# Performance work log

Hardware: AMD Instinct MI355X
Metric: run time of the kernel (lower is better)

## Reference

```python
import jax, jax.numpy as jnp
import numpy as np

N_NODES = 100000
FEAT_DIM = 256
EMBED_DIM = 256
BATCH = 50000
NUM_SAMPLE = 25
NAN_FILL = 0.01  # neigh_feats[isnan] = 0.01 in the original


def setup_inputs() -> dict:
    key = jax.random.key(0)
    k1, k2, k3, k4 = jax.random.split(key, 4)
    features = jax.random.normal(k1, (N_NODES, FEAT_DIM), dtype=jnp.float32)
    # Xavier-uniform-ish weight [embed_dim, feat_dim + embed_dim] (gcn=True)
    fan = FEAT_DIM + EMBED_DIM
    bound = float(np.sqrt(6.0 / (EMBED_DIM + fan)))
    weight = jax.random.uniform(k2, (EMBED_DIM, fan), dtype=jnp.float32,
                                minval=-bound, maxval=bound)
    nodes = jax.random.randint(k3, (BATCH,), 0, N_NODES, dtype=jnp.int64)
    neigh_idx = jax.random.randint(k4, (BATCH, NUM_SAMPLE), 0, N_NODES, dtype=jnp.int64)
    return {"features": features, "weight": weight, "nodes": nodes,
            "neigh_idx": neigh_idx}


def reference(features, weight, nodes, neigh_idx):
    # MeanAggregator: gather sampled neighbor features and mean over neighbors
    neigh_feats = features[neigh_idx].mean(axis=1)            # [B, F]
    neigh_feats = jnp.where(jnp.isnan(neigh_feats), NAN_FILL, neigh_feats)
    self_feats = features[nodes]                              # [B, F]
    combined = jnp.concatenate([self_feats, neigh_feats], axis=1)  # [B, F+E]
    # weight.matmul(combined.t()) then ReLU -> [E, B]
    out = jax.nn.relu(jnp.einsum('ef,bf->eb', weight, combined))
    return out
```

## Files before the change

kernel.cpp:

```cpp
#include <hip/hip_runtime.h>
#include <hip/hip_bf16.h>
#include <hip/hip_fp8.h>

#define FEAT    256
#define KDIM    512
#define EMBED   256
#define BATCH   50000
#define NSAMP   25
#define N_NODES 100000
#define NAN_FILL 0.01f

#define NTILE   48
#define LSTRIDE 520

typedef __attribute__((ext_vector_type(8))) short  short8;
typedef __attribute__((ext_vector_type(4))) float  floatx4;
typedef __attribute__((ext_vector_type(4))) unsigned short ushort4v;
typedef __attribute__((ext_vector_type(4))) float  float4v;

__device__ inline unsigned short f2bf(float x) {
    __hip_bfloat16 h = __float2bfloat16(x);
    union { __hip_bfloat16 h; unsigned short u; } c; c.h = h;
    return c.u;
}
__device__ inline unsigned char f2fp8(float x) {
    __hip_fp8_e4m3 t(x);
    return (unsigned char)t.__x;
}
__device__ inline float fp8f(unsigned v) {
    __hip_fp8_e4m3 t; t.__x = (unsigned char)v;
    return (float)t;
}

__global__ __launch_bounds__(256) void fconv8_kernel(
    const float* __restrict__ F, unsigned char* __restrict__ F8)
{
    const size_t i = ((size_t)blockIdx.x * 256 + threadIdx.x) * 8;
    float4v a = *(const float4v*)(F + i);
    float4v b = *(const float4v*)(F + i + 4);
    union { unsigned char c[8]; uint2 v; } o;
    o.c[0] = f2fp8(a[0]); o.c[1] = f2fp8(a[1]); o.c[2] = f2fp8(a[2]); o.c[3] = f2fp8(a[3]);
    o.c[4] = f2fp8(b[0]); o.c[5] = f2fp8(b[1]); o.c[6] = f2fp8(b[2]); o.c[7] = f2fp8(b[3]);
    *(uint2*)(F8 + i) = o.v;
}

__global__ __launch_bounds__(256) void wconv_kernel(
    const float* __restrict__ W, unsigned short* __restrict__ Wb)
{
    const int i = blockIdx.x * 256 + threadIdx.x;
    Wb[i] = f2bf(W[i]);
}

__global__ __launch_bounds__(256, 3) void enc_kernel(
    const float* __restrict__ F,
    const unsigned char* __restrict__ F8,
    const unsigned short* __restrict__ Wb,
    const int* __restrict__ nodes,
    const int* __restrict__ neigh,
    float* __restrict__ out)
{
    __shared__ unsigned short cl[NTILE * LSTRIDE];

    const int lane = threadIdx.x & 63;
    const int wave = threadIdx.x >> 6;
    const int q = lane >> 4;
    const int r = lane & 15;
    const int nbase = blockIdx.x * NTILE;

    for (int it = 0; it < NTILE / 4; ++it) {
        const int li = wave * (NTILE / 4) + it;
        int b = nbase + li;
        if (b >= BATCH) b = BATCH - 1;

        const int node = nodes[b];
        float4v sv = *(const float4v*)(F + (size_t)node * FEAT + lane * 4);

        const int* nb = neigh + (size_t)b * NSAMP;
        float s0 = 0.f, s1 = 0.f, s2 = 0.f, s3 = 0.f;
        #pragma unroll
        for (int j = 0; j < NSAMP; ++j) {
            const int idx = nb[j];
            unsigned wv = *(const unsigned*)(F8 + (size_t)idx * FEAT + lane * 4);
            s0 += fp8f(wv);
            s1 += fp8f(wv >> 8);
            s2 += fp8f(wv >> 16);
            s3 += fp8f(wv >> 24);
        }
        const float inv = 1.0f / NSAMP;
        float m0 = s0 * inv, m1 = s1 * inv, m2 = s2 * inv, m3 = s3 * inv;
        if (m0 != m0) m0 = NAN_FILL;
        if (m1 != m1) m1 = NAN_FILL;
        if (m2 != m2) m2 = NAN_FILL;
        if (m3 != m3) m3 = NAN_FILL;

        unsigned short* row = cl + li * LSTRIDE;
        ushort4v s; s[0] = f2bf(sv[0]); s[1] = f2bf(sv[1]); s[2] = f2bf(sv[2]); s[3] = f2bf(sv[3]);
        *(ushort4v*)(row + lane * 4) = s;
        ushort4v m; m[0] = f2bf(m0); m[1] = f2bf(m1); m[2] = f2bf(m2); m[3] = f2bf(m3);
        *(ushort4v*)(row + FEAT + lane * 4) = m;
    }
    __syncthreads();

    const int mbase = wave * 64;
    const short* Wp = (const short*)Wb;
    const short* cp = (const short*)cl;

    floatx4 acc[4][3] = {};

    for (int k = 0; k < KDIM; k += 32) {
        short8 afr[4], bfr[3];
        #pragma unroll
        for (int mt = 0; mt < 4; ++mt) {
            const short* p = Wp + (size_t)(mbase + mt * 16 + r) * KDIM + k + q * 8;
            afr[mt] = *(const short8*)p;
        }
        #pragma unroll
        for (int nt = 0; nt < 3; ++nt) {
            const short* p = cp + (nt * 16 + r) * LSTRIDE + k + q * 8;
            bfr[nt] = *(const short8*)p;
        }
        #pragma unroll
        for (int mt = 0; mt < 4; ++mt)
            #pragma unroll
            for (int nt = 0; nt < 3; ++nt)
                acc[mt][nt] = __builtin_amdgcn_mfma_f32_16x16x32_bf16(
                    afr[mt], bfr[nt], acc[mt][nt], 0, 0, 0);
    }

    #pragma unroll
    for (int mt = 0; mt < 4; ++mt) {
        #pragma unroll
        for (int nt = 0; nt < 3; ++nt) {
            const int col = nbase + nt * 16 + r;
            if (col < BATCH) {
                #pragma unroll
                for (int i = 0; i < 4; ++i) {
                    const int row = mbase + mt * 16 + q * 4 + i;
                    float v = acc[mt][nt][i];
                    out[(size_t)row * BATCH + col] = v > 0.f ? v : 0.f;
                }
            }
        }
    }
}

extern "C" void kernel_launch(void* const* d_in, const int* in_sizes, int n_in,
                              void* d_out, int out_size, void* d_ws, size_t ws_size,
                              hipStream_t stream) {
    const float* features = (const float*)d_in[0];
    const float* weight   = (const float*)d_in[1];
    const int*   nodes    = (const int*)d_in[2];
    const int*   neigh    = (const int*)d_in[3];
    float* out = (float*)d_out;

    unsigned char* F8  = (unsigned char*)d_ws;
    unsigned short* Wb = (unsigned short*)(F8 + (size_t)N_NODES * FEAT);

    fconv8_kernel<<<(N_NODES * FEAT) / (256 * 8), 256, 0, stream>>>(features, F8);
    wconv_kernel<<<(EMBED * KDIM) / 256, 256, 0, stream>>>(weight, Wb);

    const int nblocks = (BATCH + NTILE - 1) / NTILE;
    enc_kernel<<<nblocks, 256, 0, stream>>>(features, F8, Wb, nodes, neigh, out);
}
```

Before: 256.9 us.

## Fuse conversion kernels, use hardware packed FP8 converts, shrink node tile

The two preprocessing kernels become one launch that converts features to FP8 and the weight to BF16, with vectorized stores. Scalar FP8 encode and decode helpers are replaced by the packed hardware conversion builtins, both when converting features and when summing neighbor rows. The encoder tile shrinks from 48 to 32 nodes per block, and launch bounds request 4 blocks per CU instead of 3 to raise occupancy. The cost is more blocks and more reloads of the weight per node column.

```diff
diff --git a/kernel.cpp b/kernel.cpp
--- a/kernel.cpp
+++ b/kernel.cpp
@@ -1,6 +1,5 @@
 #include <hip/hip_runtime.h>
 #include <hip/hip_bf16.h>
-#include <hip/hip_fp8.h>
 
 #define FEAT    256
 #define KDIM    512
@@ -10,11 +9,15 @@
 #define N_NODES 100000
 #define NAN_FILL 0.01f
 
-#define NTILE   48
+#define NTILE   32
 #define LSTRIDE 520
+
+#define FCONV_BLOCKS 12500
+#define WCONV_BLOCKS 64
 
 typedef __attribute__((ext_vector_type(8))) short  short8;
 typedef __attribute__((ext_vector_type(4))) float  floatx4;
+typedef __attribute__((ext_vector_type(2))) float  float2v;
 typedef __attribute__((ext_vector_type(4))) unsigned short ushort4v;
 typedef __attribute__((ext_vector_type(4))) float  float4v;
 
@@ -23,35 +26,35 @@
     union { __hip_bfloat16 h; unsigned short u; } c; c.h = h;
     return c.u;
 }
-__device__ inline unsigned char f2fp8(float x) {
-    __hip_fp8_e4m3 t(x);
-    return (unsigned char)t.__x;
-}
-__device__ inline float fp8f(unsigned v) {
-    __hip_fp8_e4m3 t; t.__x = (unsigned char)v;
-    return (float)t;
+
+__global__ __launch_bounds__(256) void conv_kernel(
+    const float* __restrict__ F, unsigned char* __restrict__ F8,
+    const float* __restrict__ W, unsigned short* __restrict__ Wb)
+{
+    if (blockIdx.x < FCONV_BLOCKS) {
+        const size_t i = ((size_t)blockIdx.x * 256 + threadIdx.x) * 8;
+        float4v a = *(const float4v*)(F + i);
+        float4v b = *(const float4v*)(F + i + 4);
+        int p0 = 0, p1 = 0;
+        p0 = __builtin_amdgcn_cvt_pk_fp8_f32(a[0], a[1], p0, false);
+        p0 = __builtin_amdgcn_cvt_pk_fp8_f32(a[2], a[3], p0, true);
+        p1 = __builtin_amdgcn_cvt_pk_fp8_f32(b[0], b[1], p1, false);
+        p1 = __builtin_amdgcn_cvt_pk_fp8_f32(b[2], b[3], p1, true);
+        uint2 o; o.x = (unsigned)p0; o.y = (unsigned)p1;
+        *(uint2*)(F8 + i) = o;
+    } else {
+        const size_t i = ((size_t)(blockIdx.x - FCONV_BLOCKS) * 256 + threadIdx.x) * 8;
+        float4v a = *(const float4v*)(W + i);
+        float4v b = *(const float4v*)(W + i + 4);
+        ushort4v o0, o1;
+        o0[0] = f2bf(a[0]); o0[1] = f2bf(a[1]); o0[2] = f2bf(a[2]); o0[3] = f2bf(a[3]);
+        o1[0] = f2bf(b[0]); o1[1] = f2bf(b[1]); o1[2] = f2bf(b[2]); o1[3] = f2bf(b[3]);
+        *(ushort4v*)(Wb + i) = o0;
+        *(ushort4v*)(Wb + i + 4) = o1;
+    }
 }
 
-__global__ __launch_bounds__(256) void fconv8_kernel(
-    const float* __restrict__ F, unsigned char* __restrict__ F8)
-{
-    const size_t i = ((size_t)blockIdx.x * 256 + threadIdx.x) * 8;
-    float4v a = *(const float4v*)(F + i);
-    float4v b = *(const float4v*)(F + i + 4);
-    union { unsigned char c[8]; uint2 v; } o;
-    o.c[0] = f2fp8(a[0]); o.c[1] = f2fp8(a[1]); o.c[2] = f2fp8(a[2]); o.c[3] = f2fp8(a[3]);
-    o.c[4] = f2fp8(b[0]); o.c[5] = f2fp8(b[1]); o.c[6] = f2fp8(b[2]); o.c[7] = f2fp8(b[3]);
-    *(uint2*)(F8 + i) = o.v;
-}
-
-__global__ __launch_bounds__(256) void wconv_kernel(
-    const float* __restrict__ W, unsigned short* __restrict__ Wb)
-{
-    const int i = blockIdx.x * 256 + threadIdx.x;
-    Wb[i] = f2bf(W[i]);
-}
-
-__global__ __launch_bounds__(256, 3) void enc_kernel(
+__global__ __launch_bounds__(256, 4) void enc_kernel(
     const float* __restrict__ F,
     const unsigned char* __restrict__ F8,
     const unsigned short* __restrict__ Wb,
@@ -80,11 +83,10 @@
         #pragma unroll
         for (int j = 0; j < NSAMP; ++j) {
             const int idx = nb[j];
-            unsigned wv = *(const unsigned*)(F8 + (size_t)idx * FEAT + lane * 4);
-            s0 += fp8f(wv);
-            s1 += fp8f(wv >> 8);
-            s2 += fp8f(wv >> 16);
-            s3 += fp8f(wv >> 24);
+            int wv = *(const int*)(F8 + (size_t)idx * FEAT + lane * 4);
+            float2v lo = __builtin_amdgcn_cvt_pk_f32_fp8(wv, false);
+            float2v hi = __builtin_amdgcn_cvt_pk_f32_fp8(wv, true);
+            s0 += lo[0]; s1 += lo[1]; s2 += hi[0]; s3 += hi[1];
         }
         const float inv = 1.0f / NSAMP;
         float m0 = s0 * inv, m1 = s1 * inv, m2 = s2 * inv, m3 = s3 * inv;
@@ -105,24 +107,24 @@
     const short* Wp = (const short*)Wb;
     const short* cp = (const short*)cl;
 
-    floatx4 acc[4][3] = {};
+    floatx4 acc[4][2] = {};
 
     for (int k = 0; k < KDIM; k += 32) {
-        short8 afr[4], bfr[3];
+        short8 afr[4], bfr[2];
         #pragma unroll
         for (int mt = 0; mt < 4; ++mt) {
             const short* p = Wp + (size_t)(mbase + mt * 16 + r) * KDIM + k + q * 8;
             afr[mt] = *(const short8*)p;
         }
         #pragma unroll
-        for (int nt = 0; nt < 3; ++nt) {
+        for (int nt = 0; nt < 2; ++nt) {
             const short* p = cp + (nt * 16 + r) * LSTRIDE + k + q * 8;
             bfr[nt] = *(const short8*)p;
         }
         #pragma unroll
         for (int mt = 0; mt < 4; ++mt)
             #pragma unroll
-            for (int nt = 0; nt < 3; ++nt)
+            for (int nt = 0; nt < 2; ++nt)
                 acc[mt][nt] = __builtin_amdgcn_mfma_f32_16x16x32_bf16(
                     afr[mt], bfr[nt], acc[mt][nt], 0, 0, 0);
     }
@@ -130,7 +132,7 @@
     #pragma unroll
     for (int mt = 0; mt < 4; ++mt) {
         #pragma unroll
-        for (int nt = 0; nt < 3; ++nt) {
+        for (int nt = 0; nt < 2; ++nt) {
             const int col = nbase + nt * 16 + r;
             if (col < BATCH) {
                 #pragma unroll
@@ -156,8 +158,7 @@
     unsigned char* F8  = (unsigned char*)d_ws;
     unsigned short* Wb = (unsigned short*)(F8 + (size_t)N_NODES * FEAT);
 
-    fconv8_kernel<<<(N_NODES * FEAT) / (256 * 8), 256, 0, stream>>>(features, F8);
-    wconv_kernel<<<(EMBED * KDIM) / 256, 256, 0, stream>>>(weight, Wb);
+    conv_kernel<<<FCONV_BLOCKS + WCONV_BLOCKS, 256, 0, stream>>>(features, F8, weight, Wb);
 
     const int nblocks = (BATCH + NTILE - 1) / NTILE;
     enc_kernel<<<nblocks, 256, 0, stream>>>(features, F8, Wb, nodes, neigh, out);
```

Result: slower. 262.1 us (+2.0%).
